# Optimization experiments

Measured on AMD Instinct MI355X. Metric: run time of the kernel, lower is better.

## Reference

```python
import jax, jax.numpy as jnp
import numpy as np
from jax import lax

D_MODEL = 2048
D_INNER = 4096  # expand * d_model
D_CONV = 4
B, T = 4, 2048


def _rmsnorm(h):
    # F.normalize(x, dim=-1) * sqrt(D): x / max(||x||_2, 1e-12) * sqrt(D)
    n = jnp.sqrt(jnp.sum(h * h, axis=-1, keepdims=True))
    return h / jnp.maximum(n, 1e-12) * (h.shape[-1] ** 0.5)


def setup_inputs() -> dict:
    key = jax.random.key(0)
    ks = jax.random.split(key, 7)
    std = 0.02
    return {
        "x": jax.random.normal(ks[0], (B, T, D_MODEL), jnp.float32),
        "W_in": jax.random.normal(ks[1], (2 * D_INNER, D_MODEL), jnp.float32) * std,
        "conv_w": jax.random.normal(ks[2], (D_INNER, 1, D_CONV), jnp.float32) * std,
        "conv_b": jnp.zeros((D_INNER,), jnp.float32),
        "W_out": jax.random.normal(ks[3], (D_MODEL, D_INNER), jnp.float32) * std,
        "W_mlp1": jax.random.normal(ks[4], (4 * D_MODEL, D_MODEL), jnp.float32) * std,
        "W_mlp2": jax.random.normal(ks[5], (D_MODEL, 4 * D_MODEL), jnp.float32) * std,
    }


def _mamba_fallback(h, W_in, conv_w, conv_b, W_out):
    # in_proj: (B,T,D) -> (B,T,2*d_inner), split into x branch and gate z
    xz = jnp.einsum("btd,ed->bte", h, W_in)
    xp, z = jnp.split(xz, 2, axis=-1)
    # depthwise causal conv over time: torch pads (d_conv-1) both sides then slices [:T]
    # == left-pad-only causal cross-correlation
    xc = lax.conv_general_dilated(
        xp.transpose(0, 2, 1),  # (B, d_inner, T)
        conv_w,                  # (d_inner, 1, d_conv)
        window_strides=(1,),
        padding=[(D_CONV - 1, 0)],
        dimension_numbers=("NCH", "OIH", "NCH"),
        feature_group_count=D_INNER,
    ) + conv_b[None, :, None]
    xc = xc.transpose(0, 2, 1)  # (B, T, d_inner)
    y = jax.nn.silu(xc) * jax.nn.silu(z)
    return jnp.einsum("bte,de->btd", y, W_out)


def reference(x, W_in, conv_w, conv_b, W_out, W_mlp1, W_mlp2):
    # full-dimension path (active_dim=None)
    h = _rmsnorm(x)
    x = x + _mamba_fallback(h, W_in, conv_w, conv_b, W_out)
    h = _rmsnorm(x)
    m = jnp.einsum("bte,de->btd", jax.nn.relu(jnp.einsum("btd,ed->bte", h, W_mlp1)), W_mlp2)
    return x + m
```

## Files before the change

### kernel.cpp

```cpp
#include <hip/hip_runtime.h>
#include <hip/hip_bf16.h>

typedef __bf16 bf16;
typedef __bf16 bf16x8 __attribute__((ext_vector_type(8)));
typedef float f32x4 __attribute__((ext_vector_type(4)));

#define D_MODEL 2048
#define D_INNER 4096
#define ROWS    8192

__device__ __forceinline__ void gload_lds16(const void* g, void* l) {
    __builtin_amdgcn_global_load_lds(
        (const __attribute__((address_space(1))) void*)g,
        (__attribute__((address_space(3))) void*)l, 16, 0, 0);
}

__global__ __launch_bounds__(256) void f2b_kernel(const float* __restrict__ in,
                                                  bf16* __restrict__ out, int n8) {
    int i = blockIdx.x * 256 + threadIdx.x;
    if (i >= n8) return;
    long base = (long)i * 8;
    float4 a = *(const float4*)(in + base);
    float4 b = *(const float4*)(in + base + 4);
    bf16x8 o;
    o[0] = (bf16)a.x; o[1] = (bf16)a.y; o[2] = (bf16)a.z; o[3] = (bf16)a.w;
    o[4] = (bf16)b.x; o[5] = (bf16)b.y; o[6] = (bf16)b.z; o[7] = (bf16)b.w;
    *(bf16x8*)(out + base) = o;
}

__global__ __launch_bounds__(256) void rmsnorm_kernel(const float* __restrict__ x,
                                                      bf16* __restrict__ h) {
    const long row = blockIdx.x;
    const float* xr = x + row * D_MODEL;
    float4 v0 = ((const float4*)xr)[threadIdx.x * 2];
    float4 v1 = ((const float4*)xr)[threadIdx.x * 2 + 1];
    float ss = v0.x*v0.x + v0.y*v0.y + v0.z*v0.z + v0.w*v0.w
             + v1.x*v1.x + v1.y*v1.y + v1.z*v1.z + v1.w*v1.w;
    #pragma unroll
    for (int o = 32; o; o >>= 1) ss += __shfl_xor(ss, o, 64);
    __shared__ float red[4];
    if ((threadIdx.x & 63) == 0) red[threadIdx.x >> 6] = ss;
    __syncthreads();
    float tot = red[0] + red[1] + red[2] + red[3];
    float scale = 45.254834f / fmaxf(sqrtf(tot), 1e-12f);
    bf16x8 o;
    o[0] = (bf16)(v0.x*scale); o[1] = (bf16)(v0.y*scale);
    o[2] = (bf16)(v0.z*scale); o[3] = (bf16)(v0.w*scale);
    o[4] = (bf16)(v1.x*scale); o[5] = (bf16)(v1.y*scale);
    o[6] = (bf16)(v1.z*scale); o[7] = (bf16)(v1.w*scale);
    *(bf16x8*)(h + row * D_MODEL + threadIdx.x * 8) = o;
}

__global__ __launch_bounds__(256) void conv_gate_kernel(bf16* __restrict__ xz,
                                                        const float* __restrict__ cw,
                                                        const float* __restrict__ cb) {
    const int idx = blockIdx.x * 256 + threadIdx.x;
    const int c8  = idx & 511;
    const int row = idx >> 9;
    const int t   = row & 2047;
    const int c0  = c8 * 8;
    float acc[8];
    float wv[8][4];
    #pragma unroll
    for (int e = 0; e < 8; ++e) {
        float4 f = ((const float4*)cw)[c0 + e];
        wv[e][0] = f.x; wv[e][1] = f.y; wv[e][2] = f.z; wv[e][3] = f.w;
        acc[e] = cb[c0 + e];
    }
    #pragma unroll
    for (int j = 0; j < 4; ++j) {
        if (t + j - 3 >= 0) {
            bf16x8 xv = *(const bf16x8*)(xz + (long)(row + j - 3) * (2*D_INNER) + c0);
            #pragma unroll
            for (int e = 0; e < 8; ++e) acc[e] += (float)xv[e] * wv[e][j];
        }
    }
    bf16* zp = xz + (long)row * (2*D_INNER) + D_INNER + c0;
    bf16x8 zv = *(const bf16x8*)zp;
    bf16x8 yv;
    #pragma unroll
    for (int e = 0; e < 8; ++e) {
        float xc = acc[e];
        float s1 = xc / (1.f + __expf(-xc));
        float z  = (float)zv[e];
        float s2 = z / (1.f + __expf(-z));
        yv[e] = (bf16)(s1 * s2);
    }
    *(bf16x8*)zp = yv;
}

template<int EPI>
__global__ __launch_bounds__(512, 2) void gemm_bt(
        const bf16* __restrict__ A, long lda,
        const bf16* __restrict__ B,
        void* __restrict__ C, const float* __restrict__ res,
        int N, int K, int gx) {
    __shared__ __align__(16) char LB[131072];
    const int tid = threadIdx.x;
    const int w   = tid >> 6;
    const int l   = tid & 63;
    const int lr  = l & 15;

    const int nwg = gridDim.x;
    const int qq  = nwg >> 3;
    const int sw  = (blockIdx.x & 7) * qq + (blockIdx.x >> 3);
    const int bx  = sw % gx, by = sw / gx;
    const long rowBase = (long)by * 256;
    const long colBase = (long)bx * 256;

    const int srow = w * 8 + (l >> 3);
    const int schk = (l & 7) ^ ((l >> 3) & 7);
    const bf16* aSrc = A + (rowBase + srow) * lda + schk * 8;
    const bf16* bSrc = B + (colBase + srow) * (long)K + schk * 8;
    const long lda64 = 64 * lda;
    const long ldb64 = 64 * (long)K;
    const int  w1024 = w * 1024;

    auto stgA = [&](int DBB, int kt) {
        const bf16* s = aSrc + (long)kt * 64;
        gload_lds16(s,            LB + DBB +     0 + w1024);
        gload_lds16(s +   lda64,  LB + DBB +  8192 + w1024);
        gload_lds16(s + 2*lda64,  LB + DBB + 16384 + w1024);
        gload_lds16(s + 3*lda64,  LB + DBB + 24576 + w1024);
    };
    auto stgB = [&](int DBB, int kt) {
        const bf16* s = bSrc + (long)kt * 64;
        gload_lds16(s,            LB + DBB + 32768 + w1024);
        gload_lds16(s +   ldb64,  LB + DBB + 40960 + w1024);
        gload_lds16(s + 2*ldb64,  LB + DBB + 49152 + w1024);
        gload_lds16(s + 3*ldb64,  LB + DBB + 57344 + w1024);
    };

    const int cx0 = (((l >> 4)    ) ^ (l & 7)) << 4;
    const int cx1 = (((l >> 4) + 4) ^ (l & 7)) << 4;
    const int hm = w >> 2;
    const int q  = w & 3;
    int aRow[8], bRow[4];
    #pragma unroll
    for (int m = 0; m < 8; ++m) aRow[m] = hm * 16384 + (m * 16 + lr) * 128;
    #pragma unroll
    for (int n = 0; n < 4; ++n)
        bRow[n] = 32768 + (q >> 1) * 16384 + ((q & 1) * 64 + n * 16 + lr) * 128;

    const int nt  = K >> 6;
    const int nit = nt >> 1;
    f32x4 acc[8][4] = {};

    stgA(0, 0); stgB(0, 0);
    stgA(65536, 1); stgB(65536, 1);
    asm volatile("s_waitcnt vmcnt(8)" ::: "memory");
    __builtin_amdgcn_s_barrier();
    __builtin_amdgcn_sched_barrier(0);

    for (int it = 0; it < nit; ++it) {
        int kA = 2 * it + 2; if (kA >= nt) kA = 0;
        int kB = 2 * it + 3; if (kB >= nt) kB = 0;
        #pragma unroll
        for (int db = 0; db < 2; ++db) {
            const int DBB = db * 65536;
            const int kst = db ? kB : kA;
            const char* Lb = LB + DBB;
            bf16x8 aR[4][2], bL[2][2], bH[2][2];

            #pragma unroll
            for (int m = 0; m < 4; ++m) {
                aR[m][0] = *(const bf16x8*)(Lb + aRow[m] + cx0);
                aR[m][1] = *(const bf16x8*)(Lb + aRow[m] + cx1);
            }
            #pragma unroll
            for (int n = 0; n < 2; ++n) {
                bL[n][0] = *(const bf16x8*)(Lb + bRow[n] + cx0);
                bL[n][1] = *(const bf16x8*)(Lb + bRow[n] + cx1);
            }
            __builtin_amdgcn_s_barrier();
            asm volatile("s_waitcnt lgkmcnt(0)" ::: "memory");
            __builtin_amdgcn_sched_barrier(0);
            __builtin_amdgcn_s_setprio(1);
            #pragma unroll
            for (int m = 0; m < 4; ++m)
                #pragma unroll
                for (int n = 0; n < 2; ++n) {
                    acc[m][n] = __builtin_amdgcn_mfma_f32_16x16x32_bf16(aR[m][0], bL[n][0], acc[m][n], 0, 0, 0);
                    acc[m][n] = __builtin_amdgcn_mfma_f32_16x16x32_bf16(aR[m][1], bL[n][1], acc[m][n], 0, 0, 0);
                }
            __builtin_amdgcn_s_setprio(0);
            __builtin_amdgcn_s_barrier();

            #pragma unroll
            for (int n = 0; n < 2; ++n) {
                bH[n][0] = *(const bf16x8*)(Lb + bRow[n + 2] + cx0);
                bH[n][1] = *(const bf16x8*)(Lb + bRow[n + 2] + cx1);
            }
            __builtin_amdgcn_s_barrier();
            asm volatile("s_waitcnt lgkmcnt(0)" ::: "memory");
            __builtin_amdgcn_sched_barrier(0);
            __builtin_amdgcn_s_setprio(1);
            #pragma unroll
            for (int m = 0; m < 4; ++m)
                #pragma unroll
                for (int n = 0; n < 2; ++n) {
                    acc[m][n + 2] = __builtin_amdgcn_mfma_f32_16x16x32_bf16(aR[m][0], bH[n][0], acc[m][n + 2], 0, 0, 0);
                    acc[m][n + 2] = __builtin_amdgcn_mfma_f32_16x16x32_bf16(aR[m][1], bH[n][1], acc[m][n + 2], 0, 0, 0);
                }
            __builtin_amdgcn_s_setprio(0);
            __builtin_amdgcn_s_barrier();

            #pragma unroll
            for (int m = 0; m < 4; ++m) {
                aR[m][0] = *(const bf16x8*)(Lb + aRow[m + 4] + cx0);
                aR[m][1] = *(const bf16x8*)(Lb + aRow[m + 4] + cx1);
            }
            stgB(DBB, kst);
            __builtin_amdgcn_s_barrier();
            asm volatile("s_waitcnt lgkmcnt(0)" ::: "memory");
            __builtin_amdgcn_sched_barrier(0);
            __builtin_amdgcn_s_setprio(1);
            #pragma unroll
            for (int m = 0; m < 4; ++m)
                #pragma unroll
                for (int n = 0; n < 2; ++n) {
                    acc[m + 4][n + 2] = __builtin_amdgcn_mfma_f32_16x16x32_bf16(aR[m][0], bH[n][0], acc[m + 4][n + 2], 0, 0, 0);
                    acc[m + 4][n + 2] = __builtin_amdgcn_mfma_f32_16x16x32_bf16(aR[m][1], bH[n][1], acc[m + 4][n + 2], 0, 0, 0);
                }
            __builtin_amdgcn_s_setprio(0);
            __builtin_amdgcn_s_barrier();

            stgA(DBB, kst);
            __builtin_amdgcn_s_barrier();
            __builtin_amdgcn_s_setprio(1);
            #pragma unroll
            for (int m = 0; m < 4; ++m)
                #pragma unroll
                for (int n = 0; n < 2; ++n) {
                    acc[m + 4][n] = __builtin_amdgcn_mfma_f32_16x16x32_bf16(aR[m][0], bL[n][0], acc[m + 4][n], 0, 0, 0);
                    acc[m + 4][n] = __builtin_amdgcn_mfma_f32_16x16x32_bf16(aR[m][1], bL[n][1], acc[m + 4][n], 0, 0, 0);
                }
            __builtin_amdgcn_s_setprio(0);
            asm volatile("s_waitcnt vmcnt(8)" ::: "memory");
            __builtin_amdgcn_s_barrier();
        }
    }

    asm volatile("s_waitcnt vmcnt(0)" ::: "memory");

    const int lg = l >> 4;
    const long wrow = rowBase + hm * 128;
    const long wcol = colBase + q * 64;
    #pragma unroll
    for (int m = 0; m < 8; ++m) {
        #pragma unroll
        for (int n = 0; n < 4; ++n) {
            f32x4 v = acc[m][n];
            #pragma unroll
            for (int r = 0; r < 4; ++r) {
                long row = wrow + m*16 + lg*4 + r;
                long col = wcol + n*16 + lr;
                long off = row * N + col;
                if (EPI == 0)      ((bf16*)C)[off] = (bf16)v[r];
                else if (EPI == 1) ((bf16*)C)[off] = (bf16)fmaxf(v[r], 0.f);
                else               ((float*)C)[off] = res[off] + v[r];
            }
        }
    }
}

extern "C" void kernel_launch(void* const* d_in, const int* in_sizes, int n_in,
                              void* d_out, int out_size, void* d_ws, size_t ws_size,
                              hipStream_t stream) {
    const float* x      = (const float*)d_in[0];
    const float* W_in   = (const float*)d_in[1];
    const float* cw     = (const float*)d_in[2];
    const float* cb     = (const float*)d_in[3];
    const float* W_out  = (const float*)d_in[4];
    const float* W_mlp1 = (const float*)d_in[5];
    const float* W_mlp2 = (const float*)d_in[6];
    float* out = (float*)d_out;

    char* ws  = (char*)d_ws;
    bf16* wW  = (bf16*)(ws);
    bf16* h   = (bf16*)(ws + 33554432);
    bf16* xz  = (bf16*)(ws + 67108864);
    float* x2 = (float*)(ws + 201326592);
    bf16* y   = xz + D_INNER;
    bf16* m1  = xz;

    dim3 blk(256);
    dim3 gblk(512);

    f2b_kernel<<<dim3(8192), blk, 0, stream>>>(W_in, wW, 16777216/8);
    rmsnorm_kernel<<<dim3(ROWS), blk, 0, stream>>>(x, h);
    gemm_bt<0><<<dim3(1024), gblk, 0, stream>>>(h, D_MODEL, wW, xz, nullptr, 2*D_INNER, D_MODEL, 32);
    conv_gate_kernel<<<dim3(16384), blk, 0, stream>>>(xz, cw, cb);
    f2b_kernel<<<dim3(4096), blk, 0, stream>>>(W_out, wW, 8388608/8);
    gemm_bt<2><<<dim3(256), gblk, 0, stream>>>(y, 2*D_INNER, wW, x2, x, D_MODEL, D_INNER, 8);

    rmsnorm_kernel<<<dim3(ROWS), blk, 0, stream>>>(x2, h);
    f2b_kernel<<<dim3(8192), blk, 0, stream>>>(W_mlp1, wW, 16777216/8);
    gemm_bt<1><<<dim3(1024), gblk, 0, stream>>>(h, D_MODEL, wW, m1, nullptr, 4*D_MODEL, D_MODEL, 32);
    f2b_kernel<<<dim3(8192), blk, 0, stream>>>(W_mlp2, wW, 16777216/8);
    gemm_bt<2><<<dim3(256), gblk, 0, stream>>>(m1, 4*D_MODEL, wW, out, x2, D_MODEL, 4*D_MODEL, 8);
}
```

Baseline: 1.055 ms.

## Software-pipeline LDS fragment loads across K-steps and drop most GEMM barriers

Restructures the GEMM main loop so the first quadrant's A/B fragments for the next K-tile are loaded from the other LDS buffer at the end of the current step. The next step then starts MFMAs immediately, and the four per-step barriers shrink to roughly two. The intent is to cut barrier stalls and LDS-read latency exposed before each MFMA block. In exchange, fragment registers stay live across iterations and the vmcnt/barrier ordering of the async global-to-LDS stores becomes subtler, which raises race risk.

```diff
diff --git a/kernel.cpp b/kernel.cpp
--- a/kernel.cpp
+++ b/kernel.cpp
@@ -145,12 +145,37 @@
     const int nt  = K >> 6;
     const int nit = nt >> 1;
     f32x4 acc[8][4] = {};
-
-    stgA(0, 0); stgB(0, 0);
-    stgA(65536, 1); stgB(65536, 1);
+    bf16x8 AX[4][2], BL[2][2], BH[2][2];
+
+    stgB(0, 0);      stgA(0, 0);
+    stgB(65536, 1);  stgA(65536, 1);
     asm volatile("s_waitcnt vmcnt(8)" ::: "memory");
     __builtin_amdgcn_s_barrier();
     __builtin_amdgcn_sched_barrier(0);
+    #pragma unroll
+    for (int m = 0; m < 4; ++m) {
+        AX[m][0] = *(const bf16x8*)(LB + aRow[m] + cx0);
+        AX[m][1] = *(const bf16x8*)(LB + aRow[m] + cx1);
+    }
+    #pragma unroll
+    for (int n = 0; n < 2; ++n) {
+        BL[n][0] = *(const bf16x8*)(LB + bRow[n]     + cx0);
+        BL[n][1] = *(const bf16x8*)(LB + bRow[n]     + cx1);
+        BH[n][0] = *(const bf16x8*)(LB + bRow[n + 2] + cx0);
+        BH[n][1] = *(const bf16x8*)(LB + bRow[n + 2] + cx1);
+    }
+    asm volatile("s_waitcnt lgkmcnt(0)" ::: "memory");
+    __builtin_amdgcn_sched_barrier(0);
+    __builtin_amdgcn_s_setprio(1);
+    #pragma unroll
+    for (int m = 0; m < 4; ++m)
+        #pragma unroll
+        for (int n = 0; n < 2; ++n) {
+            acc[m][n] = __builtin_amdgcn_mfma_f32_16x16x32_bf16(AX[m][0], BL[n][0], acc[m][n], 0, 0, 0);
+            acc[m][n] = __builtin_amdgcn_mfma_f32_16x16x32_bf16(AX[m][1], BL[n][1], acc[m][n], 0, 0, 0);
+        }
+    __builtin_amdgcn_s_setprio(0);
+    __builtin_amdgcn_s_barrier();
 
     for (int it = 0; it < nit; ++it) {
         int kA = 2 * it + 2; if (kA >= nt) kA = 0;
@@ -158,21 +183,28 @@
         #pragma unroll
         for (int db = 0; db < 2; ++db) {
             const int DBB = db * 65536;
+            const char* Lb = LB + DBB;
+            const char* Ln = LB + (DBB ^ 65536);
             const int kst = db ? kB : kA;
-            const char* Lb = LB + DBB;
-            bf16x8 aR[4][2], bL[2][2], bH[2][2];
-
+            const bool full = (db == 0) || (it < nit - 1);
+
+            stgB(DBB, kst);
+            __builtin_amdgcn_s_setprio(1);
+            #pragma unroll
+            for (int m = 0; m < 4; ++m)
+                #pragma unroll
+                for (int n = 0; n < 2; ++n) {
+                    acc[m][n + 2] = __builtin_amdgcn_mfma_f32_16x16x32_bf16(AX[m][0], BH[n][0], acc[m][n + 2], 0, 0, 0);
+                    acc[m][n + 2] = __builtin_amdgcn_mfma_f32_16x16x32_bf16(AX[m][1], BH[n][1], acc[m][n + 2], 0, 0, 0);
+                }
+            __builtin_amdgcn_s_setprio(0);
+            asm volatile("s_waitcnt vmcnt(4)" ::: "memory");
+            __builtin_amdgcn_sched_barrier(0);
             #pragma unroll
             for (int m = 0; m < 4; ++m) {
-                aR[m][0] = *(const bf16x8*)(Lb + aRow[m] + cx0);
-                aR[m][1] = *(const bf16x8*)(Lb + aRow[m] + cx1);
+                AX[m][0] = *(const bf16x8*)(Lb + aRow[m + 4] + cx0);
+                AX[m][1] = *(const bf16x8*)(Lb + aRow[m + 4] + cx1);
             }
-            #pragma unroll
-            for (int n = 0; n < 2; ++n) {
-                bL[n][0] = *(const bf16x8*)(Lb + bRow[n] + cx0);
-                bL[n][1] = *(const bf16x8*)(Lb + bRow[n] + cx1);
-            }
-            __builtin_amdgcn_s_barrier();
             asm volatile("s_waitcnt lgkmcnt(0)" ::: "memory");
             __builtin_amdgcn_sched_barrier(0);
             __builtin_amdgcn_s_setprio(1);
@@ -180,63 +212,48 @@
             for (int m = 0; m < 4; ++m)
                 #pragma unroll
                 for (int n = 0; n < 2; ++n) {
-                    acc[m][n] = __builtin_amdgcn_mfma_f32_16x16x32_bf16(aR[m][0], bL[n][0], acc[m][n], 0, 0, 0);
-                    acc[m][n] = __builtin_amdgcn_mfma_f32_16x16x32_bf16(aR[m][1], bL[n][1], acc[m][n], 0, 0, 0);
+                    acc[m + 4][n + 2] = __builtin_amdgcn_mfma_f32_16x16x32_bf16(AX[m][0], BH[n][0], acc[m + 4][n + 2], 0, 0, 0);
+                    acc[m + 4][n + 2] = __builtin_amdgcn_mfma_f32_16x16x32_bf16(AX[m][1], BH[n][1], acc[m + 4][n + 2], 0, 0, 0);
                 }
             __builtin_amdgcn_s_setprio(0);
             __builtin_amdgcn_s_barrier();
 
-            #pragma unroll
-            for (int n = 0; n < 2; ++n) {
-                bH[n][0] = *(const bf16x8*)(Lb + bRow[n + 2] + cx0);
-                bH[n][1] = *(const bf16x8*)(Lb + bRow[n + 2] + cx1);
+            __builtin_amdgcn_s_setprio(1);
+            #pragma unroll
+            for (int m = 0; m < 4; ++m)
+                #pragma unroll
+                for (int n = 0; n < 2; ++n) {
+                    acc[m + 4][n] = __builtin_amdgcn_mfma_f32_16x16x32_bf16(AX[m][0], BL[n][0], acc[m + 4][n], 0, 0, 0);
+                    acc[m + 4][n] = __builtin_amdgcn_mfma_f32_16x16x32_bf16(AX[m][1], BL[n][1], acc[m + 4][n], 0, 0, 0);
+                }
+            __builtin_amdgcn_s_setprio(0);
+            __builtin_amdgcn_sched_barrier(0);
+            stgA(DBB, kst);
+            if (full) {
+                #pragma unroll
+                for (int m = 0; m < 4; ++m) {
+                    AX[m][0] = *(const bf16x8*)(Ln + aRow[m] + cx0);
+                    AX[m][1] = *(const bf16x8*)(Ln + aRow[m] + cx1);
+                }
+                #pragma unroll
+                for (int n = 0; n < 2; ++n) {
+                    BL[n][0] = *(const bf16x8*)(Ln + bRow[n]     + cx0);
+                    BL[n][1] = *(const bf16x8*)(Ln + bRow[n]     + cx1);
+                    BH[n][0] = *(const bf16x8*)(Ln + bRow[n + 2] + cx0);
+                    BH[n][1] = *(const bf16x8*)(Ln + bRow[n + 2] + cx1);
+                }
+                asm volatile("s_waitcnt lgkmcnt(0)" ::: "memory");
+                __builtin_amdgcn_sched_barrier(0);
+                __builtin_amdgcn_s_setprio(1);
+                #pragma unroll
+                for (int m = 0; m < 4; ++m)
+                    #pragma unroll
+                    for (int n = 0; n < 2; ++n) {
+                        acc[m][n] = __builtin_amdgcn_mfma_f32_16x16x32_bf16(AX[m][0], BL[n][0], acc[m][n], 0, 0, 0);
+                        acc[m][n] = __builtin_amdgcn_mfma_f32_16x16x32_bf16(AX[m][1], BL[n][1], acc[m][n], 0, 0, 0);
+                    }
+                __builtin_amdgcn_s_setprio(0);
             }
-            __builtin_amdgcn_s_barrier();
-            asm volatile("s_waitcnt lgkmcnt(0)" ::: "memory");
-            __builtin_amdgcn_sched_barrier(0);
-            __builtin_amdgcn_s_setprio(1);
-            #pragma unroll
-            for (int m = 0; m < 4; ++m)
-                #pragma unroll
-                for (int n = 0; n < 2; ++n) {
-                    acc[m][n + 2] = __builtin_amdgcn_mfma_f32_16x16x32_bf16(aR[m][0], bH[n][0], acc[m][n + 2], 0, 0, 0);
-                    acc[m][n + 2] = __builtin_amdgcn_mfma_f32_16x16x32_bf16(aR[m][1], bH[n][1], acc[m][n + 2], 0, 0, 0);
-                }
-            __builtin_amdgcn_s_setprio(0);
-            __builtin_amdgcn_s_barrier();
-
-            #pragma unroll
-            for (int m = 0; m < 4; ++m) {
-                aR[m][0] = *(const bf16x8*)(Lb + aRow[m + 4] + cx0);
-                aR[m][1] = *(const bf16x8*)(Lb + aRow[m + 4] + cx1);
-            }
-            stgB(DBB, kst);
-            __builtin_amdgcn_s_barrier();
-            asm volatile("s_waitcnt lgkmcnt(0)" ::: "memory");
-            __builtin_amdgcn_sched_barrier(0);
-            __builtin_amdgcn_s_setprio(1);
-            #pragma unroll
-            for (int m = 0; m < 4; ++m)
-                #pragma unroll
-                for (int n = 0; n < 2; ++n) {
-                    acc[m + 4][n + 2] = __builtin_amdgcn_mfma_f32_16x16x32_bf16(aR[m][0], bH[n][0], acc[m + 4][n + 2], 0, 0, 0);
-                    acc[m + 4][n + 2] = __builtin_amdgcn_mfma_f32_16x16x32_bf16(aR[m][1], bH[n][1], acc[m + 4][n + 2], 0, 0, 0);
-                }
-            __builtin_amdgcn_s_setprio(0);
-            __builtin_amdgcn_s_barrier();
-
-            stgA(DBB, kst);
-            __builtin_amdgcn_s_barrier();
-            __builtin_amdgcn_s_setprio(1);
-            #pragma unroll
-            for (int m = 0; m < 4; ++m)
-                #pragma unroll
-                for (int n = 0; n < 2; ++n) {
-                    acc[m + 4][n] = __builtin_amdgcn_mfma_f32_16x16x32_bf16(aR[m][0], bL[n][0], acc[m + 4][n], 0, 0, 0);
-                    acc[m + 4][n] = __builtin_amdgcn_mfma_f32_16x16x32_bf16(aR[m][1], bL[n][1], acc[m + 4][n], 0, 0, 0);
-                }
-            __builtin_amdgcn_s_setprio(0);
-            asm volatile("s_waitcnt vmcnt(8)" ::: "memory");
             __builtin_amdgcn_s_barrier();
         }
     }
```

Measured after the change: 1.007 ms. 4.6% less time.
